# Kernel tuning notes

Measured on AMD Instinct MI355X. Metric: run time of the kernel, lower is better.

## Reference

```python
import jax, jax.numpy as jnp
import numpy as np

VOCAB, EMB, HID, OUT = 4411, 64, 128, 2


def setup_inputs() -> dict:
    key = jax.random.key(0)
    ks = jax.random.split(key, 8)
    inputs = jax.random.randint(ks[0], (1024, 512), 0, VOCAB)
    s_e = 1.0
    s_ih = 1.0 / np.sqrt(HID)
    emb_table = jax.random.normal(ks[1], (VOCAB, EMB), dtype=jnp.float32) * s_e
    W_ih = jax.random.uniform(ks[2], (HID, EMB), dtype=jnp.float32, minval=-s_ih, maxval=s_ih)
    W_hh = jax.random.uniform(ks[3], (HID, HID), dtype=jnp.float32, minval=-s_ih, maxval=s_ih)
    b_ih = jax.random.uniform(ks[4], (HID,), dtype=jnp.float32, minval=-s_ih, maxval=s_ih)
    b_hh = jax.random.uniform(ks[5], (HID,), dtype=jnp.float32, minval=-s_ih, maxval=s_ih)
    s_l = 1.0 / np.sqrt(HID)
    W_lin = jax.random.uniform(ks[6], (OUT, HID), dtype=jnp.float32, minval=-s_l, maxval=s_l)
    b_lin = jax.random.uniform(ks[7], (OUT,), dtype=jnp.float32, minval=-s_l, maxval=s_l)
    return {"inputs": inputs, "emb_table": emb_table, "W_ih": W_ih, "W_hh": W_hh,
            "b_ih": b_ih, "b_hh": b_hh, "W_lin": W_lin, "b_lin": b_lin}


def reference(inputs, emb_table, W_ih, W_hh, b_ih, b_hh, W_lin, b_lin):
    # Embedding lookup: [B, T, EMB]
    emb = emb_table[inputs]
    B = emb.shape[0]
    # Precompute input projection for all timesteps: [B, T, HID]
    x_proj = jnp.einsum('bte,he->bth', emb, W_ih) + b_ih + b_hh
    h0 = jnp.zeros((B, W_hh.shape[0]), dtype=emb.dtype)

    def step(h, x_t):  # x_t: [B, HID]
        h_new = jnp.tanh(x_t + h @ W_hh.T)
        return h_new, None

    # scan over time axis
    h_final, _ = jax.lax.scan(step, h0, jnp.swapaxes(x_proj, 0, 1))
    # out_state squeeze(dim=0) -> [B, HID]; linear head -> [B, 2]
    return h_final @ W_lin.T + b_lin
```

## Files before the change

### kernel.cpp

```cpp
#include <hip/hip_runtime.h>
#include <hip/hip_bf16.h>


constexpr int Bc    = 1024;
constexpr int Tc    = 512;
constexpr int Ec    = 64;
constexpr int Hc    = 128;
constexpr int OUTc  = 2;
constexpr int VOCAB = 4411;

typedef short  short8  __attribute__((ext_vector_type(8)));
typedef float  floatx4 __attribute__((ext_vector_type(4)));

__device__ __forceinline__ unsigned short f2bf(float x) {
    union { __hip_bfloat16 h; unsigned short u; } v;
    v.h = __float2bfloat16(x);
    return v.u;
}
__device__ __forceinline__ float bf2f(unsigned short u) {
    union { float f; unsigned int u; } c;
    c.u = ((unsigned int)u) << 16;
    return c.f;
}
__device__ __forceinline__ float fast_tanh(float z) {
    const float e = __builtin_amdgcn_exp2f(2.8853900817779268f * z);
    return 1.0f - 2.0f * __builtin_amdgcn_rcpf(e + 1.0f);
}

#define LGKM_BARRIER() asm volatile("s_waitcnt lgkmcnt(0)\n\ts_barrier" ::: "memory")

constexpr int PV = 32;
__global__ __launch_bounds__(Hc) void pe_kernel(
    const float* __restrict__ emb, const float* __restrict__ W_ih,
    const float* __restrict__ b_ih, const float* __restrict__ b_hh,
    float* __restrict__ pe)
{
    const int j  = threadIdx.x;
    const int v0 = blockIdx.x * PV;

    __shared__ float es[PV * Ec];
    for (int i = j; i < PV * Ec / 4; i += Hc) {
        const int flat = i * 4, vv = flat >> 6;
        if (v0 + vv < VOCAB)
            *(float4*)&es[flat] = *(const float4*)(emb + (long)(v0 + vv) * Ec + (flat & 63));
    }

    float4 wr[Ec / 4];
#pragma unroll
    for (int e = 0; e < Ec / 4; ++e)
        wr[e] = *(const float4*)(W_ih + j * Ec + e * 4);
#pragma unroll
    for (int e = 0; e < Ec / 4; ++e)
        asm volatile("" : "+v"(wr[e].x), "+v"(wr[e].y), "+v"(wr[e].z), "+v"(wr[e].w));
    const float bias = b_ih[j] + b_hh[j];

    __syncthreads();

    for (int vv = 0; vv < PV; ++vv) {
        if (v0 + vv >= VOCAB) break;
        const float* er = &es[vv * Ec];
        float a0 = bias, a1 = 0.f, a2 = 0.f, a3 = 0.f;
#pragma unroll
        for (int e = 0; e < Ec / 4; ++e) {
            const float4 E = *(const float4*)(er + 4 * e);
            a0 = fmaf(E.x, wr[e].x, a0);
            a1 = fmaf(E.y, wr[e].y, a1);
            a2 = fmaf(E.z, wr[e].z, a2);
            a3 = fmaf(E.w, wr[e].w, a3);
        }
        pe[(long)(v0 + vv) * Hc + j] = (a0 + a1) + (a2 + a3);
    }
}

constexpr int HT_STRIDE  = 136;
constexpr int HT_BUF     = 16 * HT_STRIDE;
constexpr int TOK_STRIDE = 513;

__global__ __attribute__((amdgpu_flat_work_group_size(256, 256)))
void rnn_mfma(
    const int*   __restrict__ inputs,
    const float* __restrict__ pe,
    const float* __restrict__ W_hh,
    const float* __restrict__ W_lin,
    const float* __restrict__ b_lin,
    float* __restrict__ out)
{
    const int tid = threadIdx.x;
    const int w   = tid >> 6;
    const int L   = tid & 63;
    const int q   = L >> 4;
    const int b   = L & 15;
    const int blk = blockIdx.x;
    const int jb  = w * 32;

    __shared__ __align__(16) unsigned short HT[2 * HT_BUF];
    __shared__ int toks[16 * TOK_STRIDE];

    {
        const int base = blk * 16 * Tc;
        for (int i = tid; i < 16 * Tc / 4; i += 256) {
            const int4 v4 = *(const int4*)(inputs + base + i * 4);
            const int bb = (i * 4) >> 9, t0 = (i * 4) & 511;
            int* dst = &toks[bb * TOK_STRIDE + t0];
            dst[0] = v4.x; dst[1] = v4.y; dst[2] = v4.z; dst[3] = v4.w;
        }
    }
    {
        unsigned int* z = (unsigned int*)HT;
        for (int i = tid; i < HT_BUF / 2; i += 256) z[i] = 0u;
    }

    short8 wfrag[2][4];
#pragma unroll
    for (int jt = 0; jt < 2; ++jt) {
        const float* wr = W_hh + (jb + jt * 16 + b) * Hc;
#pragma unroll
        for (int kt = 0; kt < 4; ++kt) {
            const float4 w0 = *(const float4*)(wr + kt * 32 + q * 8);
            const float4 w1 = *(const float4*)(wr + kt * 32 + q * 8 + 4);
            union { short8 s; unsigned short u[8]; } uf;
            uf.u[0] = f2bf(w0.x); uf.u[1] = f2bf(w0.y);
            uf.u[2] = f2bf(w0.z); uf.u[3] = f2bf(w0.w);
            uf.u[4] = f2bf(w1.x); uf.u[5] = f2bf(w1.y);
            uf.u[6] = f2bf(w1.z); uf.u[7] = f2bf(w1.w);
            wfrag[jt][kt] = uf.s;
        }
    }
#pragma unroll
    for (int jt = 0; jt < 2; ++jt)
        asm volatile("" : "+v"(wfrag[jt][0]), "+v"(wfrag[jt][1]),
                          "+v"(wfrag[jt][2]), "+v"(wfrag[jt][3]));

    unsigned short* const ht0 = HT;
    unsigned short* const ht1 = HT + HT_BUF;
    int rd_off[4], wr_off[2];
#pragma unroll
    for (int kt = 0; kt < 4; ++kt)
        rd_off[kt] = b * HT_STRIDE + (kt * 4 + q) * 8;
#pragma unroll
    for (int jt = 0; jt < 2; ++jt)
        wr_off[jt] = b * HT_STRIDE + (jb + jt * 16 + q * 4);

    const int* tr = &toks[b * TOK_STRIDE];

    __syncthreads();

    float4 xpc[2], xpn[2];
    {
        const int t0 = tr[0], t1 = tr[1];
#pragma unroll
        for (int jt = 0; jt < 2; ++jt) {
            xpc[jt] = *(const float4*)(pe + (long)t0 * Hc + jb + jt * 16 + q * 4);
            xpn[jt] = *(const float4*)(pe + (long)t1 * Hc + jb + jt * 16 + q * 4);
        }
    }

    for (int t = 0; t < Tc; ++t) {
        unsigned short* const rbuf = (t & 1) ? ht1 : ht0;
        unsigned short* const wbuf = (t & 1) ? ht0 : ht1;

        short8 bfrag[4];
#pragma unroll
        for (int kt = 0; kt < 4; ++kt)
            bfrag[kt] = *(const short8*)(rbuf + rd_off[kt]);

        float4 xp2[2];
        {
            const int tk = tr[(t + 2 < Tc) ? (t + 2) : (Tc - 1)];
#pragma unroll
            for (int jt = 0; jt < 2; ++jt)
                xp2[jt] = *(const float4*)(pe + (long)tk * Hc + jb + jt * 16 + q * 4);
        }

        floatx4 acc[2];
#pragma unroll
        for (int jt = 0; jt < 2; ++jt) {
            acc[jt] = (floatx4){xpc[jt].x, xpc[jt].y, xpc[jt].z, xpc[jt].w};
#pragma unroll
            for (int kt = 0; kt < 4; ++kt)
                acc[jt] = __builtin_amdgcn_mfma_f32_16x16x32_bf16(
                    wfrag[jt][kt], bfrag[kt], acc[jt], 0, 0, 0);
        }

#pragma unroll
        for (int jt = 0; jt < 2; ++jt) {
            const float h0 = fast_tanh(acc[jt][0]);
            const float h1 = fast_tanh(acc[jt][1]);
            const float h2 = fast_tanh(acc[jt][2]);
            const float h3 = fast_tanh(acc[jt][3]);
            uint2 pk;
            pk.x = ((unsigned int)f2bf(h1) << 16) | f2bf(h0);
            pk.y = ((unsigned int)f2bf(h3) << 16) | f2bf(h2);
            *(uint2*)(wbuf + wr_off[jt]) = pk;
        }

        LGKM_BARRIER();

        xpc[0] = xpn[0]; xpc[1] = xpn[1];
        xpn[0] = xp2[0]; xpn[1] = xp2[1];
    }

    if (tid < 16 * OUTc) {
        const int bb = tid >> 1, o = tid & 1;
        float s = b_lin[o];
        const float* wl = W_lin + o * Hc;
#pragma unroll 8
        for (int k = 0; k < Hc; ++k)
            s = fmaf(bf2f(ht0[bb * HT_STRIDE + k]), wl[k], s);
        out[(blk * 16 + bb) * OUTc + o] = s;
    }
}

extern "C" void kernel_launch(void* const* d_in, const int* in_sizes, int n_in,
                              void* d_out, int out_size, void* d_ws, size_t ws_size,
                              hipStream_t stream) {
    const int*   inputs    = (const int*)d_in[0];
    const float* emb_table = (const float*)d_in[1];
    const float* W_ih      = (const float*)d_in[2];
    const float* W_hh      = (const float*)d_in[3];
    const float* b_ih      = (const float*)d_in[4];
    const float* b_hh      = (const float*)d_in[5];
    const float* W_lin     = (const float*)d_in[6];
    const float* b_lin     = (const float*)d_in[7];
    float* out = (float*)d_out;

    float* pe = (float*)d_ws;
    pe_kernel<<<(VOCAB + PV - 1) / PV, Hc, 0, stream>>>(emb_table, W_ih, b_ih, b_hh, pe);
    rnn_mfma<<<Bc / 16, 256, 0, stream>>>(inputs, pe, W_hh, W_lin, b_lin, out);
}
```

Before: 282.0 us.

## Swizzle hidden-state LDS layout, unroll time loop by two, pack bf16 pairs

Stores the hidden state in LDS in a fragment-native layout so each lane reads its MFMA B operand with one contiguous offset (L*8 + kt*512) instead of a padded row stride. The time loop is unrolled by two with ping-pong buffers and x-projection registers, which removes per-step buffer selection and register copies. MFMAs for the two output tiles are interleaved, bf16 packing uses a paired conversion intrinsic, and the pe kernel uses smaller vocabulary chunks with the register pin removed. The new layout may bring back LDS bank conflicts on the strided h writes.

```diff
diff --git a/kernel.cpp b/kernel.cpp
--- a/kernel.cpp
+++ b/kernel.cpp
@@ -22,6 +22,11 @@
     c.u = ((unsigned int)u) << 16;
     return c.f;
 }
+__device__ __forceinline__ unsigned int pack2bf(float lo, float hi) {
+    union { __hip_bfloat162 h; unsigned int u; } c;
+    c.h = __float22bfloat162_rn(float2{lo, hi});
+    return c.u;
+}
 __device__ __forceinline__ float fast_tanh(float z) {
     const float e = __builtin_amdgcn_exp2f(2.8853900817779268f * z);
     return 1.0f - 2.0f * __builtin_amdgcn_rcpf(e + 1.0f);
@@ -29,7 +34,7 @@
 
 #define LGKM_BARRIER() asm volatile("s_waitcnt lgkmcnt(0)\n\ts_barrier" ::: "memory")
 
-constexpr int PV = 32;
+constexpr int PV = 8;
 __global__ __launch_bounds__(Hc) void pe_kernel(
     const float* __restrict__ emb, const float* __restrict__ W_ih,
     const float* __restrict__ b_ih, const float* __restrict__ b_hh,
@@ -49,9 +54,6 @@
 #pragma unroll
     for (int e = 0; e < Ec / 4; ++e)
         wr[e] = *(const float4*)(W_ih + j * Ec + e * 4);
-#pragma unroll
-    for (int e = 0; e < Ec / 4; ++e)
-        asm volatile("" : "+v"(wr[e].x), "+v"(wr[e].y), "+v"(wr[e].z), "+v"(wr[e].w));
     const float bias = b_ih[j] + b_hh[j];
 
     __syncthreads();
@@ -72,8 +74,7 @@
     }
 }
 
-constexpr int HT_STRIDE  = 136;
-constexpr int HT_BUF     = 16 * HT_STRIDE;
+constexpr int HT_BUF     = 2048;
 constexpr int TOK_STRIDE = 513;
 
 __global__ __attribute__((amdgpu_flat_work_group_size(256, 256)))
@@ -133,80 +134,81 @@
 
     unsigned short* const ht0 = HT;
     unsigned short* const ht1 = HT + HT_BUF;
-    int rd_off[4], wr_off[2];
-#pragma unroll
-    for (int kt = 0; kt < 4; ++kt)
-        rd_off[kt] = b * HT_STRIDE + (kt * 4 + q) * 8;
-#pragma unroll
-    for (int jt = 0; jt < 2; ++jt)
-        wr_off[jt] = b * HT_STRIDE + (jb + jt * 16 + q * 4);
+    const int rd_base = L * 8;
+    int wr_off[2];
+#pragma unroll
+    for (int jt = 0; jt < 2; ++jt) {
+        const int j0 = jb + jt * 16 + q * 4;
+        wr_off[jt] = ((j0 >> 5) << 9) + (((j0 >> 3) & 3) * 16 + b) * 8 + (j0 & 7);
+    }
 
     const int* tr = &toks[b * TOK_STRIDE];
 
     __syncthreads();
 
-    float4 xpc[2], xpn[2];
+    float4 xpA[2], xpB[2];
+    int tk;
     {
         const int t0 = tr[0], t1 = tr[1];
+        tk = tr[2];
 #pragma unroll
         for (int jt = 0; jt < 2; ++jt) {
-            xpc[jt] = *(const float4*)(pe + (long)t0 * Hc + jb + jt * 16 + q * 4);
-            xpn[jt] = *(const float4*)(pe + (long)t1 * Hc + jb + jt * 16 + q * 4);
-        }
-    }
-
-    for (int t = 0; t < Tc; ++t) {
-        unsigned short* const rbuf = (t & 1) ? ht1 : ht0;
-        unsigned short* const wbuf = (t & 1) ? ht0 : ht1;
-
-        short8 bfrag[4];
-#pragma unroll
-        for (int kt = 0; kt < 4; ++kt)
-            bfrag[kt] = *(const short8*)(rbuf + rd_off[kt]);
-
-        float4 xp2[2];
-        {
-            const int tk = tr[(t + 2 < Tc) ? (t + 2) : (Tc - 1)];
-#pragma unroll
-            for (int jt = 0; jt < 2; ++jt)
-                xp2[jt] = *(const float4*)(pe + (long)tk * Hc + jb + jt * 16 + q * 4);
-        }
-
-        floatx4 acc[2];
-#pragma unroll
-        for (int jt = 0; jt < 2; ++jt) {
-            acc[jt] = (floatx4){xpc[jt].x, xpc[jt].y, xpc[jt].z, xpc[jt].w};
-#pragma unroll
-            for (int kt = 0; kt < 4; ++kt)
-                acc[jt] = __builtin_amdgcn_mfma_f32_16x16x32_bf16(
-                    wfrag[jt][kt], bfrag[kt], acc[jt], 0, 0, 0);
-        }
-
-#pragma unroll
-        for (int jt = 0; jt < 2; ++jt) {
-            const float h0 = fast_tanh(acc[jt][0]);
-            const float h1 = fast_tanh(acc[jt][1]);
-            const float h2 = fast_tanh(acc[jt][2]);
-            const float h3 = fast_tanh(acc[jt][3]);
-            uint2 pk;
-            pk.x = ((unsigned int)f2bf(h1) << 16) | f2bf(h0);
-            pk.y = ((unsigned int)f2bf(h3) << 16) | f2bf(h2);
-            *(uint2*)(wbuf + wr_off[jt]) = pk;
-        }
-
-        LGKM_BARRIER();
-
-        xpc[0] = xpn[0]; xpc[1] = xpn[1];
-        xpn[0] = xp2[0]; xpn[1] = xp2[1];
-    }
+            xpA[jt] = *(const float4*)(pe + (long)t0 * Hc + jb + jt * 16 + q * 4);
+            xpB[jt] = *(const float4*)(pe + (long)t1 * Hc + jb + jt * 16 + q * 4);
+        }
+    }
+
+#define RNN_STEP(T, RB, WB, XC)                                                  \
+    {                                                                            \
+        short8 bfrag[4];                                                         \
+        _Pragma("unroll")                                                        \
+        for (int kt = 0; kt < 4; ++kt)                                           \
+            bfrag[kt] = *(const short8*)((RB) + kt * 512 + rd_base);             \
+        const int tknew = tr[((T) + 3 < Tc) ? ((T) + 3) : (Tc - 1)];             \
+        floatx4 acc[2];                                                          \
+        _Pragma("unroll")                                                        \
+        for (int jt = 0; jt < 2; ++jt)                                           \
+            acc[jt] = (floatx4){XC[jt].x, XC[jt].y, XC[jt].z, XC[jt].w};         \
+        _Pragma("unroll")                                                        \
+        for (int jt = 0; jt < 2; ++jt)                                           \
+            XC[jt] = *(const float4*)(pe + (long)tk * Hc + jb + jt * 16 + q * 4);\
+        tk = tknew;                                                              \
+        _Pragma("unroll")                                                        \
+        for (int kt = 0; kt < 4; ++kt) {                                         \
+            acc[0] = __builtin_amdgcn_mfma_f32_16x16x32_bf16(                    \
+                wfrag[0][kt], bfrag[kt], acc[0], 0, 0, 0);                       \
+            acc[1] = __builtin_amdgcn_mfma_f32_16x16x32_bf16(                    \
+                wfrag[1][kt], bfrag[kt], acc[1], 0, 0, 0);                       \
+        }                                                                        \
+        _Pragma("unroll")                                                        \
+        for (int jt = 0; jt < 2; ++jt) {                                         \
+            const float h0 = fast_tanh(acc[jt][0]);                              \
+            const float h1 = fast_tanh(acc[jt][1]);                              \
+            const float h2 = fast_tanh(acc[jt][2]);                              \
+            const float h3 = fast_tanh(acc[jt][3]);                              \
+            uint2 pk;                                                            \
+            pk.x = pack2bf(h0, h1);                                              \
+            pk.y = pack2bf(h2, h3);                                              \
+            *(uint2*)((WB) + wr_off[jt]) = pk;                                   \
+        }                                                                        \
+        LGKM_BARRIER();                                                          \
+    }
+
+    for (int t = 0; t < Tc; t += 2) {
+        RNN_STEP(t,     ht0, ht1, xpA);
+        RNN_STEP(t + 1, ht1, ht0, xpB);
+    }
+#undef RNN_STEP
 
     if (tid < 16 * OUTc) {
         const int bb = tid >> 1, o = tid & 1;
         float s = b_lin[o];
         const float* wl = W_lin + o * Hc;
 #pragma unroll 8
-        for (int k = 0; k < Hc; ++k)
-            s = fmaf(bf2f(ht0[bb * HT_STRIDE + k]), wl[k], s);
+        for (int k = 0; k < Hc; ++k) {
+            const int off = ((k >> 5) << 9) + (((k >> 3) & 3) * 16 + bb) * 8 + (k & 7);
+            s = fmaf(bf2f(ht0[off]), wl[k], s);
+        }
         out[(blk * 16 + bb) * OUTc + o] = s;
     }
 }
```

Result: slower. 320.5 us (+13.7%).

## Swizzle hidden-state LDS layout, interleave MFMAs, simplify pe kernel

Applied to the files above, without the earlier changes.

Stores the hidden state in LDS in an MFMA-fragment-ordered layout, so each lane reads its B fragment with a contiguous offset (L*8 + kt*512) instead of a padded row stride. The two MFMA chains are interleaved per k-step to hide dependent-MFMA latency. The bf16 packing uses a paired conversion intrinsic. The pe precompute kernel becomes one block per vocab entry with no LDS staging, which trades reuse of W_ih in registers for more parallelism.

```diff
diff --git a/kernel.cpp b/kernel.cpp
--- a/kernel.cpp
+++ b/kernel.cpp
@@ -22,6 +22,11 @@
     c.u = ((unsigned int)u) << 16;
     return c.f;
 }
+__device__ __forceinline__ unsigned int pack2bf(float lo, float hi) {
+    union { __hip_bfloat162 h; unsigned int u; } c;
+    c.h = __float22bfloat162_rn(float2{lo, hi});
+    return c.u;
+}
 __device__ __forceinline__ float fast_tanh(float z) {
     const float e = __builtin_amdgcn_exp2f(2.8853900817779268f * z);
     return 1.0f - 2.0f * __builtin_amdgcn_rcpf(e + 1.0f);
@@ -29,51 +34,29 @@
 
 #define LGKM_BARRIER() asm volatile("s_waitcnt lgkmcnt(0)\n\ts_barrier" ::: "memory")
 
-constexpr int PV = 32;
 __global__ __launch_bounds__(Hc) void pe_kernel(
     const float* __restrict__ emb, const float* __restrict__ W_ih,
     const float* __restrict__ b_ih, const float* __restrict__ b_hh,
     float* __restrict__ pe)
 {
-    const int j  = threadIdx.x;
-    const int v0 = blockIdx.x * PV;
-
-    __shared__ float es[PV * Ec];
-    for (int i = j; i < PV * Ec / 4; i += Hc) {
-        const int flat = i * 4, vv = flat >> 6;
-        if (v0 + vv < VOCAB)
-            *(float4*)&es[flat] = *(const float4*)(emb + (long)(v0 + vv) * Ec + (flat & 63));
-    }
-
-    float4 wr[Ec / 4];
-#pragma unroll
-    for (int e = 0; e < Ec / 4; ++e)
-        wr[e] = *(const float4*)(W_ih + j * Ec + e * 4);
-#pragma unroll
-    for (int e = 0; e < Ec / 4; ++e)
-        asm volatile("" : "+v"(wr[e].x), "+v"(wr[e].y), "+v"(wr[e].z), "+v"(wr[e].w));
-    const float bias = b_ih[j] + b_hh[j];
-
-    __syncthreads();
-
-    for (int vv = 0; vv < PV; ++vv) {
-        if (v0 + vv >= VOCAB) break;
-        const float* er = &es[vv * Ec];
-        float a0 = bias, a1 = 0.f, a2 = 0.f, a3 = 0.f;
-#pragma unroll
-        for (int e = 0; e < Ec / 4; ++e) {
-            const float4 E = *(const float4*)(er + 4 * e);
-            a0 = fmaf(E.x, wr[e].x, a0);
-            a1 = fmaf(E.y, wr[e].y, a1);
-            a2 = fmaf(E.z, wr[e].z, a2);
-            a3 = fmaf(E.w, wr[e].w, a3);
-        }
-        pe[(long)(v0 + vv) * Hc + j] = (a0 + a1) + (a2 + a3);
-    }
-}
-
-constexpr int HT_STRIDE  = 136;
-constexpr int HT_BUF     = 16 * HT_STRIDE;
+    const int v = blockIdx.x;
+    const int j = threadIdx.x;
+    const float* er = emb + (long)v * Ec;
+    const float* wr = W_ih + j * Ec;
+    float a0 = b_ih[j] + b_hh[j], a1 = 0.f, a2 = 0.f, a3 = 0.f;
+#pragma unroll
+    for (int e = 0; e < Ec; e += 4) {
+        const float4 E = *(const float4*)(er + e);
+        const float4 W = *(const float4*)(wr + e);
+        a0 = fmaf(E.x, W.x, a0);
+        a1 = fmaf(E.y, W.y, a1);
+        a2 = fmaf(E.z, W.z, a2);
+        a3 = fmaf(E.w, W.w, a3);
+    }
+    pe[(long)v * Hc + j] = (a0 + a1) + (a2 + a3);
+}
+
+constexpr int HT_BUF     = 2048;
 constexpr int TOK_STRIDE = 513;
 
 __global__ __attribute__((amdgpu_flat_work_group_size(256, 256)))
@@ -133,13 +116,13 @@
 
     unsigned short* const ht0 = HT;
     unsigned short* const ht1 = HT + HT_BUF;
-    int rd_off[4], wr_off[2];
-#pragma unroll
-    for (int kt = 0; kt < 4; ++kt)
-        rd_off[kt] = b * HT_STRIDE + (kt * 4 + q) * 8;
-#pragma unroll
-    for (int jt = 0; jt < 2; ++jt)
-        wr_off[jt] = b * HT_STRIDE + (jb + jt * 16 + q * 4);
+    const int rd_base = L * 8;
+    int wr_off[2];
+#pragma unroll
+    for (int jt = 0; jt < 2; ++jt) {
+        const int j0 = jb + jt * 16 + q * 4;
+        wr_off[jt] = ((j0 >> 5) << 9) + (((j0 >> 3) & 3) * 16 + b) * 8 + (j0 & 7);
+    }
 
     const int* tr = &toks[b * TOK_STRIDE];
 
@@ -162,7 +145,7 @@
         short8 bfrag[4];
 #pragma unroll
         for (int kt = 0; kt < 4; ++kt)
-            bfrag[kt] = *(const short8*)(rbuf + rd_off[kt]);
+            bfrag[kt] = *(const short8*)(rbuf + kt * 512 + rd_base);
 
         float4 xp2[2];
         {
@@ -173,13 +156,14 @@
         }
 
         floatx4 acc[2];
-#pragma unroll
-        for (int jt = 0; jt < 2; ++jt) {
-            acc[jt] = (floatx4){xpc[jt].x, xpc[jt].y, xpc[jt].z, xpc[jt].w};
-#pragma unroll
-            for (int kt = 0; kt < 4; ++kt)
-                acc[jt] = __builtin_amdgcn_mfma_f32_16x16x32_bf16(
-                    wfrag[jt][kt], bfrag[kt], acc[jt], 0, 0, 0);
+        acc[0] = (floatx4){xpc[0].x, xpc[0].y, xpc[0].z, xpc[0].w};
+        acc[1] = (floatx4){xpc[1].x, xpc[1].y, xpc[1].z, xpc[1].w};
+#pragma unroll
+        for (int kt = 0; kt < 4; ++kt) {
+            acc[0] = __builtin_amdgcn_mfma_f32_16x16x32_bf16(
+                wfrag[0][kt], bfrag[kt], acc[0], 0, 0, 0);
+            acc[1] = __builtin_amdgcn_mfma_f32_16x16x32_bf16(
+                wfrag[1][kt], bfrag[kt], acc[1], 0, 0, 0);
         }
 
 #pragma unroll
@@ -189,8 +173,8 @@
             const float h2 = fast_tanh(acc[jt][2]);
             const float h3 = fast_tanh(acc[jt][3]);
             uint2 pk;
-            pk.x = ((unsigned int)f2bf(h1) << 16) | f2bf(h0);
-            pk.y = ((unsigned int)f2bf(h3) << 16) | f2bf(h2);
+            pk.x = pack2bf(h0, h1);
+            pk.y = pack2bf(h2, h3);
             *(uint2*)(wbuf + wr_off[jt]) = pk;
         }
 
@@ -205,8 +189,10 @@
         float s = b_lin[o];
         const float* wl = W_lin + o * Hc;
 #pragma unroll 8
-        for (int k = 0; k < Hc; ++k)
-            s = fmaf(bf2f(ht0[bb * HT_STRIDE + k]), wl[k], s);
+        for (int k = 0; k < Hc; ++k) {
+            const int off = ((k >> 5) << 9) + (((k >> 3) & 3) * 16 + bb) * 8 + (k & 7);
+            s = fmaf(bf2f(ht0[off]), wl[k], s);
+        }
         out[(blk * 16 + bb) * OUTc + o] = s;
     }
 }
@@ -225,6 +211,6 @@
     float* out = (float*)d_out;
 
     float* pe = (float*)d_ws;
-    pe_kernel<<<(VOCAB + PV - 1) / PV, Hc, 0, stream>>>(emb_table, W_ih, b_ih, b_hh, pe);
+    pe_kernel<<<VOCAB, Hc, 0, stream>>>(emb_table, W_ih, b_ih, b_hh, pe);
     rnn_mfma<<<Bc / 16, 256, 0, stream>>>(inputs, pe, W_hh, W_lin, b_lin, out);
 }
```

Result: no change. 281.5 us (-0.2%).
